# Performance work log

Measured on AMD Instinct MI355X. Metric: run time of the kernel, lower is better.

The kernel has to match this reference:

```python
import jax, jax.numpy as jnp
import numpy as np

INPUT_SIZE = 512
HIDDEN_SIZE = 1024
BATCH = 16384


def setup_inputs() -> dict:
    key = jax.random.key(0)
    ks = jax.random.split(key, 11)
    s_x = 1.0 / np.sqrt(INPUT_SIZE)
    s_h = 1.0 / np.sqrt(HIDDEN_SIZE)
    inp = {
        "x": jax.random.normal(ks[0], (BATCH, INPUT_SIZE), dtype=jnp.float32),
        "hidden": jax.random.normal(ks[1], (BATCH, HIDDEN_SIZE), dtype=jnp.float32),
        # Linear weights stored as (in, out) for x @ W
        "Wxr": jax.random.uniform(ks[2], (INPUT_SIZE, HIDDEN_SIZE), jnp.float32, -s_x, s_x),
        "bxr": jax.random.uniform(ks[3], (HIDDEN_SIZE,), jnp.float32, -s_x, s_x),
        "Whr": jax.random.uniform(ks[4], (HIDDEN_SIZE, HIDDEN_SIZE), jnp.float32, -s_h, s_h),
        "Wxz": jax.random.uniform(ks[5], (INPUT_SIZE, HIDDEN_SIZE), jnp.float32, -s_x, s_x),
        "bxz": jax.random.uniform(ks[6], (HIDDEN_SIZE,), jnp.float32, -s_x, s_x),
        "Whz": jax.random.uniform(ks[7], (HIDDEN_SIZE, HIDDEN_SIZE), jnp.float32, -s_h, s_h),
        "Wxh": jax.random.uniform(ks[8], (INPUT_SIZE, HIDDEN_SIZE), jnp.float32, -s_x, s_x),
        "bxh": jax.random.uniform(ks[9], (HIDDEN_SIZE,), jnp.float32, -s_x, s_x),
        "Whh": jax.random.uniform(ks[10], (HIDDEN_SIZE, HIDDEN_SIZE), jnp.float32, -s_h, s_h),
    }
    return inp


def reference(x, hidden, Wxr, bxr, Whr, Wxz, bxz, Whz, Wxh, bxh, Whh):
    # GRU cell, single timestep.
    r = jax.nn.sigmoid(x @ Wxr + bxr + hidden @ Whr)          # reset gate (B,H)
    z = jax.nn.sigmoid(x @ Wxz + bxz + hidden @ Whz)          # update gate (B,H)
    h_cand = jnp.tanh(x @ Wxh + bxh + (r * hidden) @ Whh)     # candidate (B,H)
    return z * hidden + (1.0 - z) * h_cand
```

## Files before the change

### kernel.cpp

```cpp
#include <hip/hip_runtime.h>

typedef unsigned short u16;
typedef unsigned int u32;
typedef __bf16 bf16x8 __attribute__((ext_vector_type(8)));
typedef float f32x4 __attribute__((ext_vector_type(4)));

#define B_ROWS 16384
#define K1 1536

__device__ __forceinline__ u16 f2bf(float f) {
  u32 u = __float_as_uint(f);
  u = (u + 0x7fffu + ((u >> 16) & 1u)) >> 16;
  return (u16)u;
}
__device__ __forceinline__ float bf2f(u16 b) {
  return __uint_as_float(((u32)b) << 16);
}
__device__ __forceinline__ void gload_lds16(const void* g, void* l) {
  __builtin_amdgcn_global_load_lds((const __attribute__((address_space(1))) void*)g,
                                   (__attribute__((address_space(3))) void*)l,
                                   16, 0, 0);
}

__global__ void cvt_xh(const float* __restrict__ x, const float* __restrict__ h,
                       u16* __restrict__ xh) {
  const int iv = blockIdx.x * 256 + threadIdx.x;
  const int row = iv / 384;
  const int col = (iv - row * 384) * 4;
  const float* src = (col < 512) ? x + (size_t)row * 512 + col
                                 : h + (size_t)row * 1024 + (col - 512);
  float4 v = *(const float4*)src;
  u32 a = (u32)f2bf(v.x) | ((u32)f2bf(v.y) << 16);
  u32 b = (u32)f2bf(v.z) | ((u32)f2bf(v.w) << 16);
  *(uint2*)(xh + (size_t)row * 1536 + col) = make_uint2(a, b);
}

__global__ void transpose_cvt6(const float* __restrict__ Wxr, const float* __restrict__ Whr,
                               const float* __restrict__ Wxz, const float* __restrict__ Whz,
                               const float* __restrict__ Wxh, const float* __restrict__ Whh,
                               u16* __restrict__ W1t, u16* __restrict__ W2t) {
  __shared__ float tile[32][33];
  const int z = blockIdx.z;
  const float* W;
  u16* T;
  int Ks, koff, roff;
  switch (z) {
    case 0:  W = Wxr; T = W1t; Ks = 512;  koff = 0;   roff = 0;    break;
    case 1:  W = Whr; T = W1t; Ks = 1024; koff = 512; roff = 0;    break;
    case 2:  W = Wxz; T = W1t; Ks = 512;  koff = 0;   roff = 1024; break;
    case 3:  W = Whz; T = W1t; Ks = 1024; koff = 512; roff = 1024; break;
    case 4:  W = Wxh; T = W2t; Ks = 512;  koff = 0;   roff = 0;    break;
    default: W = Whh; T = W2t; Ks = 1024; koff = 512; roff = 0;    break;
  }
  const int bx = blockIdx.x, by = blockIdx.y;
  if (by * 32 >= Ks) return;
  const int tx = threadIdx.x, ty = threadIdx.y;
#pragma unroll
  for (int r = 0; r < 32; r += 8)
    tile[ty + r][tx] = W[(size_t)(by * 32 + ty + r) * 1024 + bx * 32 + tx];
  __syncthreads();
#pragma unroll
  for (int r = 0; r < 32; r += 8)
    T[(size_t)(roff + bx * 32 + ty + r) * K1 + koff + by * 32 + tx] = f2bf(tile[tx][ty + r]);
}

struct Src {
  const u16 *A, *B, *A2;
  u32 sA, sB, sA2;
  int tsw;
};

__device__ __forceinline__ void gemm256(const Src& S, int nt, int brow, int bcol,
                                        u16* AsU, u16* BsU, f32x4 acc[8][4]) {
  const int tid = threadIdx.x;
  const int l = tid & 63;
  const int wid = tid >> 6;
  const int wr = wid >> 2, wc = wid & 3;
  const int lr = l & 15, kq = l >> 4;
  const int swzB = (lr & 7) * 16;
  const int kswzE = ((tid & 7) ^ ((tid >> 3) & 7)) * 8;
  const int r = tid >> 3;
  char* AsB = (char*)AsU;
  char* BsB = (char*)BsU;
  const int ldsQ = wid << 10;
  const int colK0 = (kq * 16) ^ swzB;
  const int colK1 = (64 + kq * 16) ^ swzB;
  int aRow[8], bRow[4];
#pragma unroll
  for (int m = 0; m < 8; ++m) aRow[m] = (wr * 128 + m * 16 + lr) * 128;
#pragma unroll
  for (int n = 0; n < 4; ++n) bRow[n] = (wc * 64 + n * 16 + lr) * 128;

  const u16* pA01 = S.A;
  const u16* pA23 = S.A;
  u32 offA[4], offB[4];
#pragma unroll
  for (int q = 0; q < 4; ++q) {
    offA[q] = (u32)((brow + q * 64 + r) * S.sA + kswzE) * 2u;
    offB[q] = (u32)((bcol + q * 64 + r) * S.sB + kswzE) * 2u;
  }

#define STG_A01(q_, c_) gload_lds16((const char*)pA01 + offA[q_], \
    AsB + (c_) * 32768 + (q_) * 8192 + ldsQ)
#define STG_A23(q_, c_) gload_lds16((const char*)pA23 + offA[q_], \
    AsB + (c_) * 32768 + 16384 + ((q_) - 2) * 8192 + ldsQ)
#define STG_B(q_, c_)   gload_lds16((const char*)S.B + offB[q_], \
    BsB + (c_) * 32768 + ((q_) >> 1) * 16384 + ((q_) & 1) * 8192 + ldsQ)

  STG_A01(0, 0); STG_A01(1, 0);
  STG_A23(2, 0); STG_A23(3, 0);
  STG_B(0, 0); STG_B(1, 0); STG_B(2, 0); STG_B(3, 0);
  offA[0] += 128; offA[1] += 128;
  STG_A01(0, 1); STG_A01(1, 1);
  offA[0] += 128; offA[1] += 128;
  offA[2] += 128; offA[3] += 128;
  offB[0] += 128; offB[1] += 128; offB[2] += 128; offB[3] += 128;
  asm volatile("s_waitcnt vmcnt(2)" ::: "memory");
  __builtin_amdgcn_s_barrier();
  asm volatile("" ::: "memory");

  for (int t = 0; t < nt; ++t) {
    const int c = t & 1;
    const int cb = c << 15;
    bf16x8 a[4][2], b[4][2];
#pragma unroll
    for (int m = 0; m < 4; ++m) {
      a[m][0] = *(const bf16x8*)(AsB + cb + aRow[m] + colK0);
      a[m][1] = *(const bf16x8*)(AsB + cb + aRow[m] + colK1);
    }
#pragma unroll
    for (int n = 0; n < 2; ++n) {
      b[n][0] = *(const bf16x8*)(BsB + cb + bRow[n] + colK0);
      b[n][1] = *(const bf16x8*)(BsB + cb + bRow[n] + colK1);
    }
    if (t + 1 < nt) { STG_A23(2, c ^ 1); STG_A23(3, c ^ 1); }
    __builtin_amdgcn_s_barrier();
    asm volatile("s_waitcnt lgkmcnt(0)" ::: "memory");
    __builtin_amdgcn_sched_barrier(0);
    __builtin_amdgcn_s_setprio(1);
#pragma unroll
    for (int kk = 0; kk < 2; ++kk)
#pragma unroll
      for (int m = 0; m < 4; ++m)
#pragma unroll
        for (int n = 0; n < 2; ++n)
          acc[m][n] = __builtin_amdgcn_mfma_f32_16x16x32_bf16(a[m][kk], b[n][kk], acc[m][n], 0, 0, 0);
    __builtin_amdgcn_s_setprio(0);
    __builtin_amdgcn_s_barrier();
    asm volatile("" ::: "memory");
#pragma unroll
    for (int n = 2; n < 4; ++n) {
      b[n][0] = *(const bf16x8*)(BsB + cb + bRow[n] + colK0);
      b[n][1] = *(const bf16x8*)(BsB + cb + bRow[n] + colK1);
    }
    if (t + 1 < nt) { STG_B(0, c ^ 1); STG_B(1, c ^ 1); }
    __builtin_amdgcn_s_barrier();
    asm volatile("s_waitcnt lgkmcnt(0)" ::: "memory");
    __builtin_amdgcn_sched_barrier(0);
    __builtin_amdgcn_s_setprio(1);
#pragma unroll
    for (int kk = 0; kk < 2; ++kk)
#pragma unroll
      for (int m = 0; m < 4; ++m)
#pragma unroll
        for (int n = 2; n < 4; ++n)
          acc[m][n] = __builtin_amdgcn_mfma_f32_16x16x32_bf16(a[m][kk], b[n][kk], acc[m][n], 0, 0, 0);
    __builtin_amdgcn_s_setprio(0);
    __builtin_amdgcn_s_barrier();
    asm volatile("" ::: "memory");
#pragma unroll
    for (int m = 0; m < 4; ++m) {
      a[m][0] = *(const bf16x8*)(AsB + cb + aRow[m + 4] + colK0);
      a[m][1] = *(const bf16x8*)(AsB + cb + aRow[m + 4] + colK1);
    }
    if (t + 1 < nt) { STG_B(2, c ^ 1); STG_B(3, c ^ 1); }
    __builtin_amdgcn_s_barrier();
    asm volatile("s_waitcnt lgkmcnt(0)" ::: "memory");
    __builtin_amdgcn_sched_barrier(0);
    __builtin_amdgcn_s_setprio(1);
#pragma unroll
    for (int kk = 0; kk < 2; ++kk)
#pragma unroll
      for (int m = 0; m < 4; ++m)
#pragma unroll
        for (int n = 2; n < 4; ++n)
          acc[m + 4][n] = __builtin_amdgcn_mfma_f32_16x16x32_bf16(a[m][kk], b[n][kk], acc[m + 4][n], 0, 0, 0);
    __builtin_amdgcn_s_setprio(0);
    __builtin_amdgcn_s_barrier();
    asm volatile("" ::: "memory");
    if (t + 2 < nt) { STG_A01(0, c); STG_A01(1, c); }
    __builtin_amdgcn_s_barrier();
    __builtin_amdgcn_s_setprio(1);
#pragma unroll
    for (int kk = 0; kk < 2; ++kk)
#pragma unroll
      for (int m = 0; m < 4; ++m)
#pragma unroll
        for (int n = 0; n < 2; ++n)
          acc[m + 4][n] = __builtin_amdgcn_mfma_f32_16x16x32_bf16(a[m][kk], b[n][kk], acc[m + 4][n], 0, 0, 0);
    __builtin_amdgcn_s_setprio(0);
    if (t + 2 < nt) { asm volatile("s_waitcnt vmcnt(2)" ::: "memory"); }
    else            { asm volatile("s_waitcnt vmcnt(0)" ::: "memory"); }
    __builtin_amdgcn_s_barrier();
    asm volatile("" ::: "memory");
    if (t == S.tsw - 3) {
      pA01 = S.A2;
      offA[0] = (u32)((brow + 0 * 64 + r) * S.sA2 + kswzE) * 2u;
      offA[1] = (u32)((brow + 1 * 64 + r) * S.sA2 + kswzE) * 2u;
    } else { offA[0] += 128; offA[1] += 128; }
    if (t == S.tsw - 2) {
      pA23 = S.A2;
      offA[2] = (u32)((brow + 2 * 64 + r) * S.sA2 + kswzE) * 2u;
      offA[3] = (u32)((brow + 3 * 64 + r) * S.sA2 + kswzE) * 2u;
    } else { offA[2] += 128; offA[3] += 128; }
    offB[0] += 128; offB[1] += 128; offB[2] += 128; offB[3] += 128;
  }
#undef STG_A01
#undef STG_A23
#undef STG_B
}

__global__ __launch_bounds__(512, 2) void gru_gemm1(
    const u16* __restrict__ xh, const u16* __restrict__ W1t,
    const float* __restrict__ bxr, const float* __restrict__ bxz,
    u16* __restrict__ rhb, u16* __restrict__ zb) {
  __shared__ __align__(16) u16 As[2 * 256 * 64];
  __shared__ __align__(16) u16 Bs[2 * 256 * 64];
  const int orig = blockIdx.x;
  const int slot = orig >> 3;
  const int mt = (orig & 7) + 8 * (slot >> 3);
  const int jt = slot & 7;
  const int brow = mt * 256;
  const int jcol = jt * 256;

  Src S;
  S.A = xh; S.sA = K1; S.B = W1t; S.sB = K1;
  S.A2 = xh; S.sA2 = K1; S.tsw = 1 << 20;

  f32x4 acc[8][4] = {};
  gemm256(S, 24, brow, jcol, As, Bs, acc);

  const int l = threadIdx.x & 63;
  const int wid = threadIdx.x >> 6;
  const int wr = wid >> 2, wc = wid & 3;
  const int colb = jcol + wc * 64 + (l & 15);
  const int rowb = brow + wr * 128 + (l >> 4) * 4;
  if (jt < 4) {
#pragma unroll
    for (int n = 0; n < 4; ++n) {
      const int col = colb + n * 16;
      const float bias = bxr[col];
#pragma unroll
      for (int m = 0; m < 8; ++m)
#pragma unroll
        for (int j = 0; j < 4; ++j) {
          const int row = rowb + m * 16 + j;
          const float rg = 1.f / (1.f + __expf(-(acc[m][n][j] + bias)));
          const float hv = bf2f(xh[(size_t)row * K1 + 512 + col]);
          rhb[(size_t)row * 1024 + col] = f2bf(rg * hv);
        }
    }
  } else {
#pragma unroll
    for (int n = 0; n < 4; ++n) {
      const int col = colb + n * 16 - 1024;
      const float bias = bxz[col];
#pragma unroll
      for (int m = 0; m < 8; ++m)
#pragma unroll
        for (int j = 0; j < 4; ++j) {
          const int row = rowb + m * 16 + j;
          const float zg = 1.f / (1.f + __expf(-(acc[m][n][j] + bias)));
          zb[(size_t)row * 1024 + col] = f2bf(zg);
        }
    }
  }
}

__global__ __launch_bounds__(512, 2) void gru_gemm2(
    const u16* __restrict__ xh, const u16* __restrict__ rhb,
    const u16* __restrict__ W2t, const float* __restrict__ bxh,
    const u16* __restrict__ zb, float* __restrict__ out) {
  __shared__ __align__(16) u16 As[2 * 256 * 64];
  __shared__ __align__(16) u16 Bs[2 * 256 * 64];
  const int orig = blockIdx.x;
  const int wg = (orig & 7) * 32 + (orig >> 3);
  const int mt = wg & 63, jt = wg >> 6;
  const int brow = mt * 256;
  const int jcol = jt * 256;

  Src S;
  S.A = xh; S.sA = K1; S.B = W2t; S.sB = K1;
  S.A2 = rhb; S.sA2 = 1024; S.tsw = 8;

  f32x4 acc[8][4] = {};
  gemm256(S, 24, brow, jcol, As, Bs, acc);

  const int l = threadIdx.x & 63;
  const int wid = threadIdx.x >> 6;
  const int wr = wid >> 2, wc = wid & 3;
  const int colb = jcol + wc * 64 + (l & 15);
  const int rowb = brow + wr * 128 + (l >> 4) * 4;
#pragma unroll
  for (int n = 0; n < 4; ++n) {
    const int col = colb + n * 16;
    const float bias = bxh[col];
#pragma unroll
    for (int m = 0; m < 8; ++m)
#pragma unroll
      for (int j = 0; j < 4; ++j) {
        const int row = rowb + m * 16 + j;
        const size_t idx = (size_t)row * 1024 + col;
        const float e = __expf(2.f * (acc[m][n][j] + bias));
        const float hc = 1.f - 2.f / (e + 1.f);
        const float z = bf2f(zb[idx]);
        const float h = bf2f(xh[(size_t)row * K1 + 512 + col]);
        out[idx] = z * h + (1.f - z) * hc;
      }
  }
}

extern "C" void kernel_launch(void* const* d_in, const int* in_sizes, int n_in,
                              void* d_out, int out_size, void* d_ws, size_t ws_size,
                              hipStream_t stream) {
  const float* x      = (const float*)d_in[0];
  const float* hidden = (const float*)d_in[1];
  const float* Wxr = (const float*)d_in[2];
  const float* bxr = (const float*)d_in[3];
  const float* Whr = (const float*)d_in[4];
  const float* Wxz = (const float*)d_in[5];
  const float* bxz = (const float*)d_in[6];
  const float* Whz = (const float*)d_in[7];
  const float* Wxh = (const float*)d_in[8];
  const float* bxh = (const float*)d_in[9];
  const float* Whh = (const float*)d_in[10];
  float* out = (float*)d_out;
  (void)in_sizes; (void)n_in; (void)out_size; (void)ws_size;

  char* p = (char*)d_ws;
  u16* xh  = (u16*)p; p += (size_t)B_ROWS * K1 * 2;
  u16* W1t = (u16*)p; p += (size_t)2048 * K1 * 2;
  u16* W2t = (u16*)p; p += (size_t)1024 * K1 * 2;
  u16* rhb = (u16*)p; p += (size_t)B_ROWS * 1024 * 2;
  u16* zb  = (u16*)p; p += (size_t)B_ROWS * 1024 * 2;

  cvt_xh<<<B_ROWS * 384 / 256, 256, 0, stream>>>(x, hidden, xh);
  transpose_cvt6<<<dim3(32, 32, 6), dim3(32, 8), 0, stream>>>(
      Wxr, Whr, Wxz, Whz, Wxh, Whh, W1t, W2t);

  gru_gemm1<<<512, 512, 0, stream>>>(xh, W1t, bxr, bxz, rhb, zb);
  gru_gemm2<<<256, 512, 0, stream>>>(xh, rhb, W2t, bxh, zb, out);
}
```

Baseline: 270.5 us.

## Give gemm2 its own 256x128 single-buffered kernel with more workgroups

The second GEMM no longer uses the shared double-buffered 256x256 routine. It gets a dedicated loop with 256x128 tiles, a single LDS buffer and a full vmcnt(0) wait each k-step, and the grid doubles from 256 to 512 workgroups so the GPU is better filled. The A-source switch from xh to rhb now happens inline at t==8, which lets the generic routine drop its tsw logic. The cost is that global loads no longer overlap with MFMA work, so each k-step is latency-exposed, and smaller tiles mean more total global traffic.

```diff
diff --git a/kernel.cpp b/kernel.cpp
--- a/kernel.cpp
+++ b/kernel.cpp
@@ -65,9 +65,8 @@
 }
 
 struct Src {
-  const u16 *A, *B, *A2;
-  u32 sA, sB, sA2;
-  int tsw;
+  const u16 *A, *B;
+  u32 sA, sB;
 };
 
 __device__ __forceinline__ void gemm256(const Src& S, int nt, int brow, int bcol,
@@ -91,8 +90,6 @@
 #pragma unroll
   for (int n = 0; n < 4; ++n) bRow[n] = (wc * 64 + n * 16 + lr) * 128;
 
-  const u16* pA01 = S.A;
-  const u16* pA23 = S.A;
   u32 offA[4], offB[4];
 #pragma unroll
   for (int q = 0; q < 4; ++q) {
@@ -100,9 +97,9 @@
     offB[q] = (u32)((bcol + q * 64 + r) * S.sB + kswzE) * 2u;
   }
 
-#define STG_A01(q_, c_) gload_lds16((const char*)pA01 + offA[q_], \
+#define STG_A01(q_, c_) gload_lds16((const char*)S.A + offA[q_], \
     AsB + (c_) * 32768 + (q_) * 8192 + ldsQ)
-#define STG_A23(q_, c_) gload_lds16((const char*)pA23 + offA[q_], \
+#define STG_A23(q_, c_) gload_lds16((const char*)S.A + offA[q_], \
     AsB + (c_) * 32768 + 16384 + ((q_) - 2) * 8192 + ldsQ)
 #define STG_B(q_, c_)   gload_lds16((const char*)S.B + offB[q_], \
     BsB + (c_) * 32768 + ((q_) >> 1) * 16384 + ((q_) & 1) * 8192 + ldsQ)
@@ -203,16 +200,7 @@
     else            { asm volatile("s_waitcnt vmcnt(0)" ::: "memory"); }
     __builtin_amdgcn_s_barrier();
     asm volatile("" ::: "memory");
-    if (t == S.tsw - 3) {
-      pA01 = S.A2;
-      offA[0] = (u32)((brow + 0 * 64 + r) * S.sA2 + kswzE) * 2u;
-      offA[1] = (u32)((brow + 1 * 64 + r) * S.sA2 + kswzE) * 2u;
-    } else { offA[0] += 128; offA[1] += 128; }
-    if (t == S.tsw - 2) {
-      pA23 = S.A2;
-      offA[2] = (u32)((brow + 2 * 64 + r) * S.sA2 + kswzE) * 2u;
-      offA[3] = (u32)((brow + 3 * 64 + r) * S.sA2 + kswzE) * 2u;
-    } else { offA[2] += 128; offA[3] += 128; }
+    offA[0] += 128; offA[1] += 128; offA[2] += 128; offA[3] += 128;
     offB[0] += 128; offB[1] += 128; offB[2] += 128; offB[3] += 128;
   }
 #undef STG_A01
@@ -233,10 +221,7 @@
   const int brow = mt * 256;
   const int jcol = jt * 256;
 
-  Src S;
-  S.A = xh; S.sA = K1; S.B = W1t; S.sB = K1;
-  S.A2 = xh; S.sA2 = K1; S.tsw = 1 << 20;
-
+  Src S { xh, W1t, K1, K1 };
   f32x4 acc[8][4] = {};
   gemm256(S, 24, brow, jcol, As, Bs, acc);
 
@@ -281,32 +266,95 @@
     const u16* __restrict__ xh, const u16* __restrict__ rhb,
     const u16* __restrict__ W2t, const float* __restrict__ bxh,
     const u16* __restrict__ zb, float* __restrict__ out) {
-  __shared__ __align__(16) u16 As[2 * 256 * 64];
-  __shared__ __align__(16) u16 Bs[2 * 256 * 64];
+  __shared__ __align__(16) u16 As[256 * 64];
+  __shared__ __align__(16) u16 Bs[128 * 64];
   const int orig = blockIdx.x;
-  const int wg = (orig & 7) * 32 + (orig >> 3);
-  const int mt = wg & 63, jt = wg >> 6;
+  const int wg = (orig & 7) * 64 + (orig >> 3);
+  const int mt = wg & 63;
+  const int jt = wg >> 6;
   const int brow = mt * 256;
-  const int jcol = jt * 256;
-
-  Src S;
-  S.A = xh; S.sA = K1; S.B = W2t; S.sB = K1;
-  S.A2 = rhb; S.sA2 = 1024; S.tsw = 8;
-
-  f32x4 acc[8][4] = {};
-  gemm256(S, 24, brow, jcol, As, Bs, acc);
-
-  const int l = threadIdx.x & 63;
-  const int wid = threadIdx.x >> 6;
-  const int wr = wid >> 2, wc = wid & 3;
+  const int jcol = jt * 128;
+
+  const int tid = threadIdx.x;
+  const int l = tid & 63;
+  const int wid = tid >> 6;
+  const int wrk = wid >> 1, wc = wid & 1;
+  const int lr = l & 15, kq = l >> 4;
+  const int swzB = (lr & 7) * 16;
+  const int kswzE = ((tid & 7) ^ ((tid >> 3) & 7)) * 8;
+  const int r = tid >> 3;
+  char* AsB = (char*)As;
+  char* BsB = (char*)Bs;
+  const int ldsQ = wid << 10;
+  const int colK0 = (kq * 16) ^ swzB;
+  const int colK1 = (64 + kq * 16) ^ swzB;
+  int aRow[4], bRow[4];
+#pragma unroll
+  for (int m = 0; m < 4; ++m) aRow[m] = (wrk * 64 + m * 16 + lr) * 128;
+#pragma unroll
+  for (int n = 0; n < 4; ++n) bRow[n] = (wc * 64 + n * 16 + lr) * 128;
+
+  const u16* pA = xh;
+  u32 offA[4], offB[2];
+#pragma unroll
+  for (int q = 0; q < 4; ++q) offA[q] = (u32)((brow + q * 64 + r) * K1 + kswzE) * 2u;
+#pragma unroll
+  for (int q = 0; q < 2; ++q) offB[q] = (u32)((jcol + q * 64 + r) * K1 + kswzE) * 2u;
+
+  f32x4 acc[4][4] = {};
+  for (int t = 0; t < 24; ++t) {
+    if (t == 8) {
+      pA = rhb;
+#pragma unroll
+      for (int q = 0; q < 4; ++q) offA[q] = (u32)((brow + q * 64 + r) * 1024 + kswzE) * 2u;
+    }
+#pragma unroll
+    for (int q = 0; q < 4; ++q)
+      gload_lds16((const char*)pA + offA[q], AsB + q * 8192 + ldsQ);
+#pragma unroll
+    for (int q = 0; q < 2; ++q)
+      gload_lds16((const char*)W2t + offB[q], BsB + q * 8192 + ldsQ);
+    asm volatile("s_waitcnt vmcnt(0)" ::: "memory");
+    __builtin_amdgcn_s_barrier();
+    asm volatile("" ::: "memory");
+    bf16x8 a[4][2], b[4][2];
+#pragma unroll
+    for (int n = 0; n < 4; ++n) {
+      b[n][0] = *(const bf16x8*)(BsB + bRow[n] + colK0);
+      b[n][1] = *(const bf16x8*)(BsB + bRow[n] + colK1);
+    }
+#pragma unroll
+    for (int m = 0; m < 4; ++m) {
+      a[m][0] = *(const bf16x8*)(AsB + aRow[m] + colK0);
+      a[m][1] = *(const bf16x8*)(AsB + aRow[m] + colK1);
+    }
+    asm volatile("s_waitcnt lgkmcnt(0)" ::: "memory");
+    __builtin_amdgcn_sched_barrier(0);
+    __builtin_amdgcn_s_setprio(1);
+#pragma unroll
+    for (int kk = 0; kk < 2; ++kk)
+#pragma unroll
+      for (int m = 0; m < 4; ++m)
+#pragma unroll
+        for (int n = 0; n < 4; ++n)
+          acc[m][n] = __builtin_amdgcn_mfma_f32_16x16x32_bf16(a[m][kk], b[n][kk], acc[m][n], 0, 0, 0);
+    __builtin_amdgcn_s_setprio(0);
+    __builtin_amdgcn_s_barrier();
+    asm volatile("" ::: "memory");
+#pragma unroll
+    for (int q = 0; q < 4; ++q) offA[q] += 128;
+#pragma unroll
+    for (int q = 0; q < 2; ++q) offB[q] += 128;
+  }
+
   const int colb = jcol + wc * 64 + (l & 15);
-  const int rowb = brow + wr * 128 + (l >> 4) * 4;
+  const int rowb = brow + wrk * 64 + (l >> 4) * 4;
 #pragma unroll
   for (int n = 0; n < 4; ++n) {
     const int col = colb + n * 16;
     const float bias = bxh[col];
 #pragma unroll
-    for (int m = 0; m < 8; ++m)
+    for (int m = 0; m < 4; ++m)
 #pragma unroll
       for (int j = 0; j < 4; ++j) {
         const int row = rowb + m * 16 + j;
@@ -349,5 +397,5 @@
       Wxr, Whr, Wxz, Whz, Wxh, Whh, W1t, W2t);
 
   gru_gemm1<<<512, 512, 0, stream>>>(xh, W1t, bxr, bxz, rhb, zb);
-  gru_gemm2<<<256, 512, 0, stream>>>(xh, rhb, W2t, bxh, zb, out);
-}
+  gru_gemm2<<<512, 512, 0, stream>>>(xh, rhb, W2t, bxh, zb, out);
+}
```

Result: slower. 304.2 us (+12.5%).
